# Kernel tuning notes

Hardware: AMD Instinct MI355X
Metric: run time of the kernel (lower is better)

## Reference

```python
import jax, jax.numpy as jnp
import numpy as np

B = 65536
E = 8          # king buckets / experts
IN = 640
H = 256


def setup_inputs() -> dict:
    key = jax.random.key(0)
    ks = jax.random.split(key, 12)
    inp = {
        "white_features": jax.random.uniform(ks[0], (B, IN), dtype=jnp.float32),
        "black_features": jax.random.uniform(ks[1], (B, IN), dtype=jnp.float32),
        "white_bucket": jax.random.randint(ks[2], (B,), 0, E, dtype=jnp.int32),
        "black_bucket": jax.random.randint(ks[3], (B,), 0, E, dtype=jnp.int32),
        "stm": jax.random.uniform(ks[4], (B,), dtype=jnp.float32),
        "W_ft": jax.random.normal(ks[5], (E, H, IN), dtype=jnp.float32) * 0.1,
        # output MLP: Linear(512,32) -> ReLU -> Linear(32,32) -> ReLU -> Linear(32,1)
        "W1": jax.random.normal(ks[6], (32, 2 * H), dtype=jnp.float32) * float(np.sqrt(2.0 / (32 + 2 * H))),
        "b1": jnp.zeros((32,), dtype=jnp.float32),
        "W2": jax.random.normal(ks[7], (32, 32), dtype=jnp.float32) * float(np.sqrt(2.0 / 64)),
        "b2": jnp.zeros((32,), dtype=jnp.float32),
        "W3": jax.random.normal(ks[8], (1, 32), dtype=jnp.float32) * float(np.sqrt(2.0 / 33)),
        "b3": jnp.zeros((1,), dtype=jnp.float32),
    }
    return inp


def _bucketed_transform(x, bucket, W_ft):
    # Route each sample to its expert: compute all 8 small GEMMs, select via one-hot.
    # beh intermediate [B, E, H] avoids the huge gathered-weight tensor [B, H, IN].
    sel = jax.nn.one_hot(bucket % E, E, dtype=x.dtype)          # [B, E]
    h = jnp.einsum('bi,ehi,be->bh', x, W_ft, sel)               # [B, H]
    return jax.nn.relu(h)


def reference(white_features, black_features, white_bucket, black_bucket, stm,
              W_ft, W1, b1, W2, b2, W3, b3):
    wh = _bucketed_transform(white_features, white_bucket, W_ft)   # [B, 256]
    bh = _bucketed_transform(black_features, black_bucket, W_ft)   # [B, 256]
    c = jnp.concatenate([wh, bh], axis=1)                          # [B, 512]
    h = jax.nn.relu(c @ W1.T + b1)
    h = jax.nn.relu(h @ W2.T + b2)
    out = h @ W3.T + b3                                            # [B, 1]
    return out * stm[:, None]
```

## Files before the change

kernel.cpp:

```cpp
#include <hip/hip_runtime.h>


#define NB 65536
#define NIN 640
#define NH 256
#define NE 8
#define PB 128
#define NPERM (2*NB + NE*PB)
#define N_WFT (NE*NH*NIN)
#define N_W1  (32*512)

typedef _Float16 f16_t;
typedef f16_t f16x8 __attribute__((ext_vector_type(8)));
typedef float f32x4 __attribute__((ext_vector_type(4)));

__global__ void k_init(const float* __restrict__ Wft, const float* __restrict__ W1,
                       f16_t* __restrict__ Whf, f16_t* __restrict__ W1h,
                       int* __restrict__ hdr, int* __restrict__ perm)
{
    int idx = blockIdx.x * 256 + threadIdx.x;
    int stride = gridDim.x * 256;
    for (int i = idx; i < N_WFT / 8; i += stride) {
        const float4* src = (const float4*)Wft + (size_t)i * 2;
        float4 v0 = src[0], v1 = src[1];
        f16x8 h;
        h[0]=(f16_t)v0.x; h[1]=(f16_t)v0.y; h[2]=(f16_t)v0.z; h[3]=(f16_t)v0.w;
        h[4]=(f16_t)v1.x; h[5]=(f16_t)v1.y; h[6]=(f16_t)v1.z; h[7]=(f16_t)v1.w;
        *((f16x8*)Whf + i) = h;
    }
    for (int i = idx; i < N_W1 / 8; i += stride) {
        const float4* src = (const float4*)W1 + (size_t)i * 2;
        float4 v0 = src[0], v1 = src[1];
        f16x8 h;
        h[0]=(f16_t)v0.x; h[1]=(f16_t)v0.y; h[2]=(f16_t)v0.z; h[3]=(f16_t)v0.w;
        h[4]=(f16_t)v1.x; h[5]=(f16_t)v1.y; h[6]=(f16_t)v1.z; h[7]=(f16_t)v1.w;
        *((f16x8*)W1h + i) = h;
    }
    for (int i = idx; i < NPERM; i += stride) perm[i] = -1;
    if (idx < 64) hdr[idx] = 0;
}

__global__ void k_hist(const int* __restrict__ wb, const int* __restrict__ bb,
                       int* __restrict__ hdr)
{
    __shared__ int lcnt[8];
    const int tid = threadIdx.x;
    if (tid < 8) lcnt[tid] = 0;
    __syncthreads();
    int i = blockIdx.x * 256 + tid;
    int b = (i < NB ? wb[i] : bb[i - NB]) & 7;
    atomicAdd(&lcnt[b], 1);
    __syncthreads();
    if (tid < 8 && lcnt[tid] > 0) atomicAdd(&hdr[tid], lcnt[tid]);
}

__global__ void k_prefix(int* __restrict__ hdr)
{
    if (threadIdx.x == 0 && blockIdx.x == 0) {
        int* cnt  = hdr;
        int* pofs = hdr + 8;
        int* cur  = hdr + 17;
        int acc = 0;
        for (int e = 0; e < 8; ++e) {
            pofs[e] = acc; cur[e] = acc;
            acc += ((cnt[e] + PB - 1) / PB) * PB;
        }
        pofs[8] = acc;
    }
}

__global__ void k_scatter(const int* __restrict__ wb, const int* __restrict__ bb,
                          int* __restrict__ hdr, int* __restrict__ perm)
{
    __shared__ int lcnt[8];
    __shared__ int lbase[8];
    const int tid = threadIdx.x;
    if (tid < 8) lcnt[tid] = 0;
    __syncthreads();
    int i = blockIdx.x * 256 + tid;
    int b = (i < NB ? wb[i] : bb[i - NB]) & 7;
    int rank = atomicAdd(&lcnt[b], 1);
    __syncthreads();
    if (tid < 8) lbase[tid] = lcnt[tid] ? atomicAdd(&hdr[17 + tid], lcnt[tid]) : 0;
    __syncthreads();
    perm[lbase[b] + rank] = i;
}

__global__ __launch_bounds__(512, 2)
void k_gemm(const float* __restrict__ wf, const float* __restrict__ bfeat,
            const f16_t* __restrict__ Whf, const int* __restrict__ hdr,
            const int* __restrict__ perm, f16_t* __restrict__ cbuf)
{
    __shared__ f16_t As[128 * 64];
    __shared__ f16_t Bs[256 * 64];
    __shared__ int rowids[128];

    const int tid = threadIdx.x;
    const int slot0 = blockIdx.x * PB;

    const int* pofs = hdr + 8;
    const int total = pofs[8];
    if (slot0 >= total) return;
    int e = 0;
    #pragma unroll
    for (int i = 1; i < 8; ++i) if (slot0 >= pofs[i]) e = i;

    if (tid < 128) rowids[tid] = perm[slot0 + tid];
    __syncthreads();

    const f16_t* We = Whf + (size_t)e * (NH * NIN);

    f32x4 acc[4][4];
    #pragma unroll
    for (int m = 0; m < 4; ++m)
        #pragma unroll
        for (int n = 0; n < 4; ++n) acc[m][n] = (f32x4){0.f, 0.f, 0.f, 0.f};

    const int wid = tid >> 6;
    const int lane = tid & 63;
    const int wr = wid >> 2, wc = wid & 3;
    const int l15 = lane & 15, l4 = lane >> 4;

    for (int ks = 0; ks < NIN / 64; ++ks) {
        const int k0 = ks * 64;
        __syncthreads();
        {
            const int kg = tid & 7;
            const int rbase = tid >> 3;
            #pragma unroll
            for (int p = 0; p < 2; ++p) {
                int row = rbase + p * 64;
                int r = rowids[row];
                float4 v0 = {0.f,0.f,0.f,0.f}, v1 = {0.f,0.f,0.f,0.f};
                if (r >= 0) {
                    const float* src = (r < NB ? wf + (size_t)r * NIN
                                               : bfeat + (size_t)(r - NB) * NIN) + k0 + kg * 8;
                    v0 = *(const float4*)(src);
                    v1 = *(const float4*)(src + 4);
                }
                f16x8 h;
                h[0]=(f16_t)v0.x; h[1]=(f16_t)v0.y; h[2]=(f16_t)v0.z; h[3]=(f16_t)v0.w;
                h[4]=(f16_t)v1.x; h[5]=(f16_t)v1.y; h[6]=(f16_t)v1.z; h[7]=(f16_t)v1.w;
                int byte = (row * 64 + kg * 8) * 2;
                *(f16x8*)((char*)As + (byte ^ ((row & 7) << 4))) = h;
            }
        }
        {
            const int kg = tid & 7;
            const int nbase = tid >> 3;
            #pragma unroll
            for (int p = 0; p < 4; ++p) {
                int n = nbase + p * 64;
                f16x8 h = *(const f16x8*)(We + (size_t)n * NIN + k0 + kg * 8);
                int byte = (n * 64 + kg * 8) * 2;
                *(f16x8*)((char*)Bs + (byte ^ ((n & 7) << 4))) = h;
            }
        }
        __syncthreads();
        #pragma unroll
        for (int kk = 0; kk < 2; ++kk) {
            f16x8 af[4], bfr[4];
            const int kidx = kk * 32 + l4 * 8;
            #pragma unroll
            for (int m = 0; m < 4; ++m) {
                int row = wr * 64 + m * 16 + l15;
                int byte = (row * 64 + kidx) * 2;
                af[m] = *(const f16x8*)((const char*)As + (byte ^ ((row & 7) << 4)));
            }
            #pragma unroll
            for (int n = 0; n < 4; ++n) {
                int col = wc * 64 + n * 16 + l15;
                int byte = (col * 64 + kidx) * 2;
                bfr[n] = *(const f16x8*)((const char*)Bs + (byte ^ ((col & 7) << 4)));
            }
            #pragma unroll
            for (int m = 0; m < 4; ++m)
                #pragma unroll
                for (int n = 0; n < 4; ++n)
                    acc[m][n] = __builtin_amdgcn_mfma_f32_16x16x32_f16(af[m], bfr[n], acc[m][n], 0, 0, 0);
        }
    }

    #pragma unroll
    for (int m = 0; m < 4; ++m) {
        #pragma unroll
        for (int j = 0; j < 4; ++j) {
            int row = wr * 64 + m * 16 + l4 * 4 + j;
            int r = rowids[row];
            if (r < 0) continue;
            size_t drow; int coff;
            if (r < NB) { drow = r; coff = 0; } else { drow = r - NB; coff = 256; }
            f16_t* dst = cbuf + drow * 512 + coff + wc * 64 + l15;
            #pragma unroll
            for (int n = 0; n < 4; ++n) {
                float v = acc[m][n][j];
                v = v > 0.f ? v : 0.f;
                dst[n * 16] = (f16_t)v;
            }
        }
    }
}

__global__ __launch_bounds__(256, 2)
void k_mlp(const f16_t* __restrict__ cbuf, const f16_t* __restrict__ W1h,
           const float* __restrict__ b1, const float* __restrict__ W2,
           const float* __restrict__ b2, const float* __restrict__ W3,
           const float* __restrict__ b3, const float* __restrict__ stm,
           float* __restrict__ out)
{
    __shared__ f16_t cs[64 * 512];
    __shared__ float h1s[64][33];

    const int tid = threadIdx.x;
    const int s0 = blockIdx.x * 64;

    #pragma unroll
    for (int it = 0; it < 16; ++it) {
        int idx = it * 256 + tid;
        int row = idx >> 6;
        int tr = idx & 63;
        f16x8 v = *(const f16x8*)(cbuf + (size_t)(s0 + row) * 512 + tr * 8);
        int byte = (row * 512 + tr * 8) * 2;
        *(f16x8*)((char*)cs + (byte ^ ((row & 7) << 4))) = v;
    }
    __syncthreads();

    const int wid = tid >> 6, lane = tid & 63;
    const int l15 = lane & 15, l4 = lane >> 4;
    f32x4 acc0 = (f32x4){0.f,0.f,0.f,0.f};
    f32x4 acc1 = (f32x4){0.f,0.f,0.f,0.f};
    #pragma unroll 4
    for (int ks = 0; ks < 16; ++ks) {
        int k = ks * 32 + l4 * 8;
        int row = wid * 16 + l15;
        int byte = (row * 512 + k) * 2;
        f16x8 a  = *(const f16x8*)((const char*)cs + (byte ^ ((row & 7) << 4)));
        f16x8 b0 = *(const f16x8*)(W1h + (size_t)l15 * 512 + k);
        f16x8 b1v = *(const f16x8*)(W1h + (size_t)(16 + l15) * 512 + k);
        acc0 = __builtin_amdgcn_mfma_f32_16x16x32_f16(a, b0, acc0, 0, 0, 0);
        acc1 = __builtin_amdgcn_mfma_f32_16x16x32_f16(a, b1v, acc1, 0, 0, 0);
    }
    #pragma unroll
    for (int j = 0; j < 4; ++j) {
        int srow = wid * 16 + l4 * 4 + j;
        float v0 = acc0[j] + b1[l15];
        float v1 = acc1[j] + b1[16 + l15];
        h1s[srow][l15]      = v0 > 0.f ? v0 : 0.f;
        h1s[srow][16 + l15] = v1 > 0.f ? v1 : 0.f;
    }
    __syncthreads();

    const int s_in = lane >> 2, q = lane & 3;
    const int srow = wid * 16 + s_in;
    float h2[8];
    #pragma unroll
    for (int n = 0; n < 8; ++n) {
        int nn = q * 8 + n;
        float sum = b2[nn];
        #pragma unroll
        for (int k = 0; k < 32; ++k) sum += W2[nn * 32 + k] * h1s[srow][k];
        h2[n] = sum > 0.f ? sum : 0.f;
    }
    float p = 0.f;
    #pragma unroll
    for (int n = 0; n < 8; ++n) p += W3[q * 8 + n] * h2[n];
    p += __shfl_xor(p, 1);
    p += __shfl_xor(p, 2);
    if (q == 0) {
        out[s0 + srow] = (p + b3[0]) * stm[s0 + srow];
    }
}

extern "C" void kernel_launch(void* const* d_in, const int* in_sizes, int n_in,
                              void* d_out, int out_size, void* d_ws, size_t ws_size,
                              hipStream_t stream)
{
    const float* wf    = (const float*)d_in[0];
    const float* bfeat = (const float*)d_in[1];
    const int*   wb    = (const int*)d_in[2];
    const int*   bb    = (const int*)d_in[3];
    const float* stm   = (const float*)d_in[4];
    const float* Wft   = (const float*)d_in[5];
    const float* W1    = (const float*)d_in[6];
    const float* b1    = (const float*)d_in[7];
    const float* W2    = (const float*)d_in[8];
    const float* b2    = (const float*)d_in[9];
    const float* W3    = (const float*)d_in[10];
    const float* b3    = (const float*)d_in[11];
    float* out = (float*)d_out;

    char* ws = (char*)d_ws;
    int*   hdr  = (int*)ws;
    int*   perm = (int*)(ws + 256);
    f16_t* Whf  = (f16_t*)(ws + 528640);
    f16_t* W1h  = (f16_t*)(ws + 3150080);
    f16_t* cbuf = (f16_t*)(ws + 3182848);

    k_init   <<<512, 256, 0, stream>>>(Wft, W1, Whf, W1h, hdr, perm);
    k_hist   <<<512, 256, 0, stream>>>(wb, bb, hdr);
    k_prefix <<<1,   64,  0, stream>>>(hdr);
    k_scatter<<<512, 256, 0, stream>>>(wb, bb, hdr, perm);
    k_gemm   <<<NPERM / PB, 512, 0, stream>>>(wf, bfeat, Whf, hdr, perm, cbuf);
    k_mlp    <<<NB / 64, 256, 0, stream>>>(cbuf, W1h, b1, W2, b2, W3, b3, stm, out);
}
```

Measured before the change: 472.8 us.

## Prefetch next A tile into registers and raise gemm occupancy hint

```diff
diff --git a/kernel.cpp b/kernel.cpp
--- a/kernel.cpp
+++ b/kernel.cpp
@@ -86,7 +86,7 @@
     perm[lbase[b] + rank] = i;
 }
 
-__global__ __launch_bounds__(512, 2)
+__global__ __launch_bounds__(512, 4)
 void k_gemm(const float* __restrict__ wf, const float* __restrict__ bfeat,
             const f16_t* __restrict__ Whf, const int* __restrict__ hdr,
             const int* __restrict__ perm, f16_t* __restrict__ cbuf)
@@ -110,6 +110,27 @@
 
     const f16_t* We = Whf + (size_t)e * (NH * NIN);
 
+    const int kg = tid & 7;
+    const int rbase = tid >> 3;
+    const float* asrc[2];
+    int abyte[2];
+    #pragma unroll
+    for (int p = 0; p < 2; ++p) {
+        int row = rbase + p * 64;
+        int r = rowids[row];
+        asrc[p] = (r < 0) ? nullptr
+                : (r < NB ? wf + (size_t)r * NIN
+                          : bfeat + (size_t)(r - NB) * NIN) + kg * 8;
+        abyte[p] = ((row * 64 + kg * 8) * 2) ^ ((row & 7) << 4);
+    }
+    const f16_t* bsrc = We + (size_t)rbase * NIN + kg * 8;
+    int bbyte[4];
+    #pragma unroll
+    for (int p = 0; p < 4; ++p) {
+        int n = rbase + p * 64;
+        bbyte[p] = ((n * 64 + kg * 8) * 2) ^ ((n & 7) << 4);
+    }
+
     f32x4 acc[4][4];
     #pragma unroll
     for (int m = 0; m < 4; ++m)
@@ -121,42 +142,37 @@
     const int wr = wid >> 2, wc = wid & 3;
     const int l15 = lane & 15, l4 = lane >> 4;
 
+    float4 pa0[2], pa1[2];
+    #pragma unroll
+    for (int p = 0; p < 2; ++p) {
+        pa0[p] = (float4){0.f,0.f,0.f,0.f};
+        pa1[p] = (float4){0.f,0.f,0.f,0.f};
+        if (asrc[p]) { pa0[p] = *(const float4*)(asrc[p]);
+                       pa1[p] = *(const float4*)(asrc[p] + 4); }
+    }
+
     for (int ks = 0; ks < NIN / 64; ++ks) {
         const int k0 = ks * 64;
+        #pragma unroll
+        for (int p = 0; p < 2; ++p) {
+            f16x8 h;
+            h[0]=(f16_t)pa0[p].x; h[1]=(f16_t)pa0[p].y; h[2]=(f16_t)pa0[p].z; h[3]=(f16_t)pa0[p].w;
+            h[4]=(f16_t)pa1[p].x; h[5]=(f16_t)pa1[p].y; h[6]=(f16_t)pa1[p].z; h[7]=(f16_t)pa1[p].w;
+            *(f16x8*)((char*)As + abyte[p]) = h;
+        }
+        #pragma unroll
+        for (int p = 0; p < 4; ++p) {
+            f16x8 hb = *(const f16x8*)(bsrc + (size_t)p * 64 * NIN + k0);
+            *(f16x8*)((char*)Bs + bbyte[p]) = hb;
+        }
         __syncthreads();
-        {
-            const int kg = tid & 7;
-            const int rbase = tid >> 3;
+        if (ks < NIN / 64 - 1) {
             #pragma unroll
             for (int p = 0; p < 2; ++p) {
-                int row = rbase + p * 64;
-                int r = rowids[row];
-                float4 v0 = {0.f,0.f,0.f,0.f}, v1 = {0.f,0.f,0.f,0.f};
-                if (r >= 0) {
-                    const float* src = (r < NB ? wf + (size_t)r * NIN
-                                               : bfeat + (size_t)(r - NB) * NIN) + k0 + kg * 8;
-                    v0 = *(const float4*)(src);
-                    v1 = *(const float4*)(src + 4);
-                }
-                f16x8 h;
-                h[0]=(f16_t)v0.x; h[1]=(f16_t)v0.y; h[2]=(f16_t)v0.z; h[3]=(f16_t)v0.w;
-                h[4]=(f16_t)v1.x; h[5]=(f16_t)v1.y; h[6]=(f16_t)v1.z; h[7]=(f16_t)v1.w;
-                int byte = (row * 64 + kg * 8) * 2;
-                *(f16x8*)((char*)As + (byte ^ ((row & 7) << 4))) = h;
+                if (asrc[p]) { pa0[p] = *(const float4*)(asrc[p] + k0 + 64);
+                               pa1[p] = *(const float4*)(asrc[p] + k0 + 68); }
             }
         }
-        {
-            const int kg = tid & 7;
-            const int nbase = tid >> 3;
-            #pragma unroll
-            for (int p = 0; p < 4; ++p) {
-                int n = nbase + p * 64;
-                f16x8 h = *(const f16x8*)(We + (size_t)n * NIN + k0 + kg * 8);
-                int byte = (n * 64 + kg * 8) * 2;
-                *(f16x8*)((char*)Bs + (byte ^ ((n & 7) << 4))) = h;
-            }
-        }
-        __syncthreads();
         #pragma unroll
         for (int kk = 0; kk < 2; ++kk) {
             f16x8 af[4], bfr[4];
@@ -179,6 +195,7 @@
                 for (int n = 0; n < 4; ++n)
                     acc[m][n] = __builtin_amdgcn_mfma_f32_16x16x32_f16(af[m], bfr[n], acc[m][n], 0, 0, 0);
         }
+        __syncthreads();
     }
 
     #pragma unroll
```

Result: no change. 475.7 us (+0.6%).

## Replace LDS-tiled expert GEMM with per-wave direct-global MFMA streaming

Applied to the files above, without the earlier changes.

```diff
diff --git a/kernel.cpp b/kernel.cpp
--- a/kernel.cpp
+++ b/kernel.cpp
@@ -86,17 +86,13 @@
     perm[lbase[b] + rank] = i;
 }
 
-__global__ __launch_bounds__(512, 2)
+__global__ __launch_bounds__(256, 3)
 void k_gemm(const float* __restrict__ wf, const float* __restrict__ bfeat,
             const f16_t* __restrict__ Whf, const int* __restrict__ hdr,
             const int* __restrict__ perm, f16_t* __restrict__ cbuf)
 {
-    __shared__ f16_t As[128 * 64];
-    __shared__ f16_t Bs[256 * 64];
-    __shared__ int rowids[128];
-
-    const int tid = threadIdx.x;
-    const int slot0 = blockIdx.x * PB;
+    const int tid = threadIdx.x;
+    const int slot0 = blockIdx.x * 64;
 
     const int* pofs = hdr + 8;
     const int total = pofs[8];
@@ -105,98 +101,54 @@
     #pragma unroll
     for (int i = 1; i < 8; ++i) if (slot0 >= pofs[i]) e = i;
 
-    if (tid < 128) rowids[tid] = perm[slot0 + tid];
-    __syncthreads();
-
     const f16_t* We = Whf + (size_t)e * (NH * NIN);
-
-    f32x4 acc[4][4];
-    #pragma unroll
-    for (int m = 0; m < 4; ++m)
-        #pragma unroll
-        for (int n = 0; n < 4; ++n) acc[m][n] = (f32x4){0.f, 0.f, 0.f, 0.f};
 
     const int wid = tid >> 6;
     const int lane = tid & 63;
-    const int wr = wid >> 2, wc = wid & 3;
     const int l15 = lane & 15, l4 = lane >> 4;
-
-    for (int ks = 0; ks < NIN / 64; ++ks) {
-        const int k0 = ks * 64;
-        __syncthreads();
-        {
-            const int kg = tid & 7;
-            const int rbase = tid >> 3;
-            #pragma unroll
-            for (int p = 0; p < 2; ++p) {
-                int row = rbase + p * 64;
-                int r = rowids[row];
-                float4 v0 = {0.f,0.f,0.f,0.f}, v1 = {0.f,0.f,0.f,0.f};
-                if (r >= 0) {
-                    const float* src = (r < NB ? wf + (size_t)r * NIN
-                                               : bfeat + (size_t)(r - NB) * NIN) + k0 + kg * 8;
-                    v0 = *(const float4*)(src);
-                    v1 = *(const float4*)(src + 4);
-                }
-                f16x8 h;
-                h[0]=(f16_t)v0.x; h[1]=(f16_t)v0.y; h[2]=(f16_t)v0.z; h[3]=(f16_t)v0.w;
-                h[4]=(f16_t)v1.x; h[5]=(f16_t)v1.y; h[6]=(f16_t)v1.z; h[7]=(f16_t)v1.w;
-                int byte = (row * 64 + kg * 8) * 2;
-                *(f16x8*)((char*)As + (byte ^ ((row & 7) << 4))) = h;
-            }
-        }
-        {
-            const int kg = tid & 7;
-            const int nbase = tid >> 3;
-            #pragma unroll
-            for (int p = 0; p < 4; ++p) {
-                int n = nbase + p * 64;
-                f16x8 h = *(const f16x8*)(We + (size_t)n * NIN + k0 + kg * 8);
-                int byte = (n * 64 + kg * 8) * 2;
-                *(f16x8*)((char*)Bs + (byte ^ ((n & 7) << 4))) = h;
-            }
-        }
-        __syncthreads();
+    const int rowbase = slot0 + wid * 16;
+
+    const int rA = perm[rowbase + l15];
+    const float* aptr = (rA < 0) ? nullptr
+                      : (rA < NB ? wf + (size_t)rA * NIN
+                                 : bfeat + (size_t)(rA - NB) * NIN) + l4 * 8;
+    const f16_t* bptr = We + (size_t)l15 * NIN + l4 * 8;
+
+    f32x4 acc[16];
+    #pragma unroll
+    for (int n = 0; n < 16; ++n) acc[n] = (f32x4){0.f, 0.f, 0.f, 0.f};
+
+    float4 p0 = {0.f,0.f,0.f,0.f}, p1 = {0.f,0.f,0.f,0.f};
+    if (aptr) { p0 = *(const float4*)(aptr); p1 = *(const float4*)(aptr + 4); }
+
+    for (int kk = 0; kk < NIN / 32; ++kk) {
+        f16x8 af;
+        af[0]=(f16_t)p0.x; af[1]=(f16_t)p0.y; af[2]=(f16_t)p0.z; af[3]=(f16_t)p0.w;
+        af[4]=(f16_t)p1.x; af[5]=(f16_t)p1.y; af[6]=(f16_t)p1.z; af[7]=(f16_t)p1.w;
+        if (kk < NIN / 32 - 1 && aptr) {
+            p0 = *(const float4*)(aptr + (kk + 1) * 32);
+            p1 = *(const float4*)(aptr + (kk + 1) * 32 + 4);
+        }
+        const f16_t* bk = bptr + kk * 32;
         #pragma unroll
-        for (int kk = 0; kk < 2; ++kk) {
-            f16x8 af[4], bfr[4];
-            const int kidx = kk * 32 + l4 * 8;
-            #pragma unroll
-            for (int m = 0; m < 4; ++m) {
-                int row = wr * 64 + m * 16 + l15;
-                int byte = (row * 64 + kidx) * 2;
-                af[m] = *(const f16x8*)((const char*)As + (byte ^ ((row & 7) << 4)));
-            }
-            #pragma unroll
-            for (int n = 0; n < 4; ++n) {
-                int col = wc * 64 + n * 16 + l15;
-                int byte = (col * 64 + kidx) * 2;
-                bfr[n] = *(const f16x8*)((const char*)Bs + (byte ^ ((col & 7) << 4)));
-            }
-            #pragma unroll
-            for (int m = 0; m < 4; ++m)
-                #pragma unroll
-                for (int n = 0; n < 4; ++n)
-                    acc[m][n] = __builtin_amdgcn_mfma_f32_16x16x32_f16(af[m], bfr[n], acc[m][n], 0, 0, 0);
-        }
-    }
-
-    #pragma unroll
-    for (int m = 0; m < 4; ++m) {
+        for (int n = 0; n < 16; ++n) {
+            f16x8 bfr = *(const f16x8*)(bk + (size_t)n * 16 * NIN);
+            acc[n] = __builtin_amdgcn_mfma_f32_16x16x32_f16(af, bfr, acc[n], 0, 0, 0);
+        }
+    }
+
+    #pragma unroll
+    for (int j = 0; j < 4; ++j) {
+        int r = perm[rowbase + l4 * 4 + j];
+        if (r < 0) continue;
+        size_t drow; int coff;
+        if (r < NB) { drow = r; coff = 0; } else { drow = r - NB; coff = 256; }
+        f16_t* dst = cbuf + drow * 512 + coff + l15;
         #pragma unroll
-        for (int j = 0; j < 4; ++j) {
-            int row = wr * 64 + m * 16 + l4 * 4 + j;
-            int r = rowids[row];
-            if (r < 0) continue;
-            size_t drow; int coff;
-            if (r < NB) { drow = r; coff = 0; } else { drow = r - NB; coff = 256; }
-            f16_t* dst = cbuf + drow * 512 + coff + wc * 64 + l15;
-            #pragma unroll
-            for (int n = 0; n < 4; ++n) {
-                float v = acc[m][n][j];
-                v = v > 0.f ? v : 0.f;
-                dst[n * 16] = (f16_t)v;
-            }
+        for (int n = 0; n < 16; ++n) {
+            float v = acc[n][j];
+            v = v > 0.f ? v : 0.f;
+            dst[n * 16] = (f16_t)v;
         }
     }
 }
@@ -300,6 +252,6 @@
     k_hist   <<<512, 256, 0, stream>>>(wb, bb, hdr);
     k_prefix <<<1,   64,  0, stream>>>(hdr);
     k_scatter<<<512, 256, 0, stream>>>(wb, bb, hdr, perm);
-    k_gemm   <<<NPERM / PB, 512, 0, stream>>>(wf, bfeat, Whf, hdr, perm, cbuf);
+    k_gemm   <<<NPERM / 64, 256, 0, stream>>>(wf, bfeat, Whf, hdr, perm, cbuf);
     k_mlp    <<<NB / 64, 256, 0, stream>>>(cbuf, W1h, b1, W2, b2, W3, b3, stm, out);
 }
```

Result: slower. 743.2 us (+57.2%).

## Double-buffer GEMM LDS tiles with async global_load_lds for weights

Applied to the files above, without the earlier changes.

```diff
diff --git a/kernel.cpp b/kernel.cpp
--- a/kernel.cpp
+++ b/kernel.cpp
@@ -86,13 +86,80 @@
     perm[lbase[b] + rank] = i;
 }
 
+
+#define STAGE_B(kt, c) do {                                                     \
+    _Pragma("unroll")                                                           \
+    for (int i_ = 0; i_ < 4; ++i_) {                                            \
+        int qq = wid * 4 + i_;                                                  \
+        int n_ = qq * 8 + (lane >> 3);                                          \
+        const f16_t* srcB = We + (size_t)n_ * NIN + (kt) * 64                   \
+                            + 8 * ((lane & 7) ^ (n_ & 7));                      \
+        char* dstB = (char*)(&Bs[c][0]) + qq * 1024;                            \
+        __builtin_amdgcn_global_load_lds(                                       \
+            (const __attribute__((address_space(1))) void*)srcB,                \
+            (__attribute__((address_space(3))) void*)dstB, 16, 0, 0);           \
+    }                                                                           \
+} while (0)
+
+#define ISSUE_A(P0, P1, kt) do {                                                \
+    _Pragma("unroll")                                                           \
+    for (int p_ = 0; p_ < 2; ++p_) {                                            \
+        P0[p_] = (float4){0.f,0.f,0.f,0.f};                                     \
+        P1[p_] = (float4){0.f,0.f,0.f,0.f};                                     \
+        if (asrc[p_]) {                                                         \
+            P0[p_] = *(const float4*)(asrc[p_] + (kt) * 64);                    \
+            P1[p_] = *(const float4*)(asrc[p_] + (kt) * 64 + 4);                \
+        }                                                                       \
+    }                                                                           \
+} while (0)
+
+#define CVT_WRITE_A(P0, P1, c) do {                                             \
+    _Pragma("unroll")                                                           \
+    for (int p_ = 0; p_ < 2; ++p_) {                                            \
+        f16x8 h;                                                                \
+        h[0]=(f16_t)P0[p_].x; h[1]=(f16_t)P0[p_].y;                             \
+        h[2]=(f16_t)P0[p_].z; h[3]=(f16_t)P0[p_].w;                             \
+        h[4]=(f16_t)P1[p_].x; h[5]=(f16_t)P1[p_].y;                             \
+        h[6]=(f16_t)P1[p_].z; h[7]=(f16_t)P1[p_].w;                             \
+        *(f16x8*)((char*)(&As[c][0]) + abyte[p_]) = h;                          \
+    }                                                                           \
+} while (0)
+
+#define COMPUTE(c) do {                                                         \
+    _Pragma("unroll")                                                           \
+    for (int kk = 0; kk < 2; ++kk) {                                            \
+        f16x8 af[4], bfr[4];                                                    \
+        const int kidx = kk * 32 + l4 * 8;                                      \
+        _Pragma("unroll")                                                       \
+        for (int m = 0; m < 4; ++m) {                                           \
+            int row = wr * 64 + m * 16 + l15;                                   \
+            int byte = (row * 64 + kidx) * 2;                                   \
+            af[m] = *(const f16x8*)((const char*)(&As[c][0])                    \
+                                    + (byte ^ ((row & 7) << 4)));               \
+        }                                                                       \
+        _Pragma("unroll")                                                       \
+        for (int n = 0; n < 4; ++n) {                                           \
+            int col = wc * 64 + n * 16 + l15;                                   \
+            int byte = (col * 64 + kidx) * 2;                                   \
+            bfr[n] = *(const f16x8*)((const char*)(&Bs[c][0])                   \
+                                     + (byte ^ ((col & 7) << 4)));              \
+        }                                                                       \
+        _Pragma("unroll")                                                       \
+        for (int m = 0; m < 4; ++m)                                             \
+            _Pragma("unroll")                                                   \
+            for (int n = 0; n < 4; ++n)                                         \
+                acc[m][n] = __builtin_amdgcn_mfma_f32_16x16x32_f16(             \
+                    af[m], bfr[n], acc[m][n], 0, 0, 0);                         \
+    }                                                                           \
+} while (0)
+
 __global__ __launch_bounds__(512, 2)
 void k_gemm(const float* __restrict__ wf, const float* __restrict__ bfeat,
             const f16_t* __restrict__ Whf, const int* __restrict__ hdr,
             const int* __restrict__ perm, f16_t* __restrict__ cbuf)
 {
-    __shared__ f16_t As[128 * 64];
-    __shared__ f16_t Bs[256 * 64];
+    __shared__ f16_t As[2][128 * 64];
+    __shared__ f16_t Bs[2][256 * 64];
     __shared__ int rowids[128];
 
     const int tid = threadIdx.x;
@@ -110,75 +177,53 @@
 
     const f16_t* We = Whf + (size_t)e * (NH * NIN);
 
-    f32x4 acc[4][4];
-    #pragma unroll
-    for (int m = 0; m < 4; ++m)
-        #pragma unroll
-        for (int n = 0; n < 4; ++n) acc[m][n] = (f32x4){0.f, 0.f, 0.f, 0.f};
-
     const int wid = tid >> 6;
     const int lane = tid & 63;
     const int wr = wid >> 2, wc = wid & 3;
     const int l15 = lane & 15, l4 = lane >> 4;
 
-    for (int ks = 0; ks < NIN / 64; ++ks) {
-        const int k0 = ks * 64;
+    const int kg = tid & 7;
+    const int rbase = tid >> 3;
+    const float* asrc[2];
+    int abyte[2];
+    #pragma unroll
+    for (int p = 0; p < 2; ++p) {
+        int row = rbase + p * 64;
+        int r = rowids[row];
+        asrc[p] = (r < 0) ? nullptr
+                : (r < NB ? wf + (size_t)r * NIN
+                          : bfeat + (size_t)(r - NB) * NIN) + kg * 8;
+        abyte[p] = ((row * 64 + kg * 8) * 2) ^ ((row & 7) << 4);
+    }
+
+    f32x4 acc[4][4];
+    #pragma unroll
+    for (int m = 0; m < 4; ++m)
+        #pragma unroll
+        for (int n = 0; n < 4; ++n) acc[m][n] = (f32x4){0.f, 0.f, 0.f, 0.f};
+
+    float4 paE0[2], paE1[2], paO0[2], paO1[2];
+
+    ISSUE_A(paE0, paE1, 0);
+    ISSUE_A(paO0, paO1, 1);
+    STAGE_B(0, 0);
+    CVT_WRITE_A(paE0, paE1, 0);
+    __syncthreads();
+
+    #pragma unroll
+    for (int dt = 0; dt < 5; ++dt) {
+        STAGE_B(2 * dt + 1, 1);
+        if (dt < 4) ISSUE_A(paE0, paE1, 2 * dt + 2);
+        CVT_WRITE_A(paO0, paO1, 1);
+        COMPUTE(0);
         __syncthreads();
-        {
-            const int kg = tid & 7;
-            const int rbase = tid >> 3;
-            #pragma unroll
-            for (int p = 0; p < 2; ++p) {
-                int row = rbase + p * 64;
-                int r = rowids[row];
-                float4 v0 = {0.f,0.f,0.f,0.f}, v1 = {0.f,0.f,0.f,0.f};
-                if (r >= 0) {
-                    const float* src = (r < NB ? wf + (size_t)r * NIN
-                                               : bfeat + (size_t)(r - NB) * NIN) + k0 + kg * 8;
-                    v0 = *(const float4*)(src);
-                    v1 = *(const float4*)(src + 4);
-                }
-                f16x8 h;
-                h[0]=(f16_t)v0.x; h[1]=(f16_t)v0.y; h[2]=(f16_t)v0.z; h[3]=(f16_t)v0.w;
-                h[4]=(f16_t)v1.x; h[5]=(f16_t)v1.y; h[6]=(f16_t)v1.z; h[7]=(f16_t)v1.w;
-                int byte = (row * 64 + kg * 8) * 2;
-                *(f16x8*)((char*)As + (byte ^ ((row & 7) << 4))) = h;
-            }
+        if (dt < 4) {
+            STAGE_B(2 * dt + 2, 0);
+            ISSUE_A(paO0, paO1, 2 * dt + 3);
+            CVT_WRITE_A(paE0, paE1, 0);
         }
-        {
-            const int kg = tid & 7;
-            const int nbase = tid >> 3;
-            #pragma unroll
-            for (int p = 0; p < 4; ++p) {
-                int n = nbase + p * 64;
-                f16x8 h = *(const f16x8*)(We + (size_t)n * NIN + k0 + kg * 8);
-                int byte = (n * 64 + kg * 8) * 2;
-                *(f16x8*)((char*)Bs + (byte ^ ((n & 7) << 4))) = h;
-            }
-        }
+        COMPUTE(1);
         __syncthreads();
-        #pragma unroll
-        for (int kk = 0; kk < 2; ++kk) {
-            f16x8 af[4], bfr[4];
-            const int kidx = kk * 32 + l4 * 8;
-            #pragma unroll
-            for (int m = 0; m < 4; ++m) {
-                int row = wr * 64 + m * 16 + l15;
-                int byte = (row * 64 + kidx) * 2;
-                af[m] = *(const f16x8*)((const char*)As + (byte ^ ((row & 7) << 4)));
-            }
-            #pragma unroll
-            for (int n = 0; n < 4; ++n) {
-                int col = wc * 64 + n * 16 + l15;
-                int byte = (col * 64 + kidx) * 2;
-                bfr[n] = *(const f16x8*)((const char*)Bs + (byte ^ ((col & 7) << 4)));
-            }
-            #pragma unroll
-            for (int m = 0; m < 4; ++m)
-                #pragma unroll
-                for (int n = 0; n < 4; ++n)
-                    acc[m][n] = __builtin_amdgcn_mfma_f32_16x16x32_f16(af[m], bfr[n], acc[m][n], 0, 0, 0);
-        }
     }
 
     #pragma unroll
```

After: 481.7 us. No clear change (+1.9%).
